# Performance work log

Hardware: AMD Instinct MI355X
Metric: run time of the kernel (lower is better)

Reference implementation:

```python
import jax, jax.numpy as jnp
import numpy as np

KH = KW = 3
PAD = 1


def _conv2d(x, w, b):
    y = jax.lax.conv_general_dilated(
        x, w, window_strides=(1, 1), padding=((PAD, PAD), (PAD, PAD)),
        dimension_numbers=("NCHW", "OIHW", "NCHW"))
    return y + b[None, :, None, None]


def _bilinear_sample_one(img, ys, xs):
    # img: [C,H,W]; ys,xs: [K,h,w] absolute sampling coords; zeros outside.
    C, H, W = img.shape
    flat = img.reshape(C, H * W)
    y0 = jnp.floor(ys)
    x0 = jnp.floor(xs)
    wy = ys - y0
    wx = xs - x0

    def gather(yi, xi):
        valid = (yi >= 0) & (yi <= H - 1) & (xi >= 0) & (xi <= W - 1)
        yc = jnp.clip(yi, 0, H - 1).astype(jnp.int32)
        xc = jnp.clip(xi, 0, W - 1).astype(jnp.int32)
        idx = (yc * W + xc).reshape(-1)
        v = jnp.take(flat, idx, axis=1).reshape((C,) + yi.shape)
        return v * valid.astype(img.dtype)

    v00 = gather(y0, x0)
    v01 = gather(y0, x0 + 1)
    v10 = gather(y0 + 1, x0)
    v11 = gather(y0 + 1, x0 + 1)
    return (v00 * (1 - wy) * (1 - wx) + v01 * (1 - wy) * wx
            + v10 * wy * (1 - wx) + v11 * wy * wx)  # [C,K,h,w]


def deform_conv2d(x, offset, weight, bias):
    # x: [B,C,H,W]; offset: [B,2K,h,w] with (dy,dx) per tap; stride 1, pad 1.
    B, C, H, W = x.shape
    h, w = offset.shape[2], offset.shape[3]
    K = KH * KW
    off = offset.reshape(B, K, 2, h, w)
    ky = (jnp.arange(K) // KW - PAD).astype(x.dtype)  # tap row displacement
    kx = (jnp.arange(K) % KW - PAD).astype(x.dtype)
    ii = jnp.arange(h, dtype=x.dtype)[None, :, None]
    jj = jnp.arange(w, dtype=x.dtype)[None, None, :]
    ys = ii - PAD + ky[:, None, None] + off[:, :, 0]  # [B,K,h,w]
    xs = jj - PAD + kx[:, None, None] + off[:, :, 1]
    sampled = jax.vmap(_bilinear_sample_one)(x, ys, xs)  # [B,C,K,h,w]
    Co = weight.shape[0]
    out = jnp.einsum('ock,bckhw->bohw', weight.reshape(Co, C, K), sampled)
    return out + bias[None, :, None, None]


def setup_inputs() -> dict:
    key = jax.random.key(0)
    ks = jax.random.split(key, 5)
    B, C, H, W = 4, 64, 128, 128
    x = jax.random.normal(ks[0], (B, C, H, W), dtype=jnp.float32)
    w_off = jax.random.normal(ks[1], (4, C, KH, KW), dtype=jnp.float32) * 0.05
    b_off = jnp.zeros((4,), dtype=jnp.float32)
    weight = jax.random.normal(ks[2], (C, C, KH, KW), dtype=jnp.float32) * 0.05
    bias = jnp.zeros((C,), dtype=jnp.float32)
    # base_offset: canonical 3x3 tap displacements, layout (dy,dx) per tap.
    ky = np.repeat(np.arange(KH) - PAD, KW).astype(np.float32)
    kx = np.tile(np.arange(KW) - PAD, KH).astype(np.float32)
    base = np.stack([ky, kx], axis=1).reshape(-1)  # [18]
    base_offset = jnp.asarray(np.broadcast_to(base[None, :, None, None], (1, 18, H, W)).copy())
    idx = np.arange(18)
    mask1 = jnp.asarray(idx % 2 == 0)  # y coords -> scale1
    mask2 = jnp.asarray(idx % 2 == 1)  # x coords -> scale2
    return {"x": x, "w_off": w_off, "b_off": b_off, "weight": weight,
            "bias": bias, "base_offset": base_offset, "mask1": mask1, "mask2": mask2}


def reference(x, w_off, b_off, weight, bias, base_offset, mask1, mask2):
    off = _conv2d(x, w_off, b_off)  # [B,4,h,w]
    scale1 = jax.nn.relu(off[:, 2:3]) + 1.0  # [B,1,h,w]
    scale2 = jax.nn.relu(off[:, 3:4]) + 1.0
    shift = jnp.tile(off[:, :2], (1, KH * KW, 1, 1))  # [B,18,h,w]
    # scaled_offset[:, mask1] = base*scale1 ; scaled_offset[:, mask2] = base*scale2
    scale_full = jnp.where(mask1[None, :, None, None], scale1, scale2)  # [B,18,h,w]
    offset = base_offset * scale_full - base_offset + shift
    return deform_conv2d(x, offset, weight, bias)
```

## Files before the change

kernel.cpp:

```cpp
#include <hip/hip_runtime.h>

#define Hd 128
#define Wd 128
#define Cd 64
#define COd 64
#define Bd 4
#define HWd (Hd*Wd)

typedef __attribute__((ext_vector_type(8))) short  short8;
typedef __attribute__((ext_vector_type(4))) float  f32x4;
typedef __attribute__((ext_vector_type(2))) float  f32x2;

__device__ __align__(16) short g_wbf[COd*576];
__device__ __align__(16) short g_woffbf[16*576];
__device__ float4 g_offs[Bd*HWd];
__device__ __align__(16) unsigned short g_xt[(size_t)Bd*HWd*Cd];

static __device__ __forceinline__ unsigned short f2bf(float v) {
    unsigned u = __float_as_uint(v);
    u += 0x7FFFu + ((u >> 16) & 1u);
    return (unsigned short)(u >> 16);
}
static __device__ __forceinline__ f32x2 bf2(unsigned u) {
    return (f32x2){__uint_as_float(u << 16), __uint_as_float(u & 0xFFFF0000u)};
}
static __device__ __forceinline__ unsigned cvtpk(float lo, float hi) {
    unsigned r;
    asm("v_cvt_pk_bf16_f32 %0, %1, %2" : "=v"(r) : "v"(lo), "v"(hi));
    return r;
}

__global__ __launch_bounds__(256) void k_prep(const float* __restrict__ x,
                                              const float* __restrict__ weight,
                                              const float* __restrict__ w_off) {
    int bid = blockIdx.x;
    if (bid < 512) {
        int b = bid >> 7, y = bid & 127;
        int px = threadIdx.x & 127;
        int h  = threadIdx.x >> 7;
        const float* xb = x + (size_t)b*Cd*HWd + y*Wd + px;
        unsigned short* ob = g_xt + ((size_t)(b*HWd) + y*Wd + px)*Cd + h*32;
        #pragma unroll
        for (int oct = 0; oct < 4; ++oct) {
            unsigned pk[4];
            #pragma unroll
            for (int e = 0; e < 4; ++e) {
                float v0 = xb[(size_t)(h*32 + oct*8 + 2*e    )*HWd];
                float v1 = xb[(size_t)(h*32 + oct*8 + 2*e + 1)*HWd];
                pk[e] = (unsigned)f2bf(v0) | ((unsigned)f2bf(v1) << 16);
            }
            *(uint4*)(ob + oct*8) = make_uint4(pk[0], pk[1], pk[2], pk[3]);
        }
    } else if (bid < 656) {
        int g = (bid - 512)*256 + threadIdx.x;
        if (g < COd*576) {
            int co = g / 576, k = g % 576;
            int t = k >> 6, c = k & 63;
            g_wbf[g] = (short)f2bf(weight[(co*Cd + c)*9 + t]);
        }
    } else {
        int g = (bid - 656)*256 + threadIdx.x;
        if (g < 16*576) {
            int row = g / 576, k = g % 576;
            int t = k >> 6, c = k & 63;
            g_woffbf[g] = (row < 4) ? (short)f2bf(w_off[(row*Cd + c)*9 + t]) : (short)0;
        }
    }
}

__global__ __launch_bounds__(256) void k_offs(const float* __restrict__ b_off) {
    int orig = blockIdx.x;
    int xcd = orig & 7, slot = orig >> 3;
    int g = xcd*2 + (slot >> 6);
    int s = slot & 63;
    int b  = g >> 2;
    int i  = (g & 3)*32 + (s >> 1);
    int j0 = (s & 1) << 6;

    int w  = threadIdx.x >> 6;
    int l  = threadIdx.x & 63;
    int pc = l & 15, q = l >> 4;
    int j  = j0 + w*16 + pc;

    const unsigned short* xb = g_xt + (size_t)b*HWd*Cd;
    const short* arow = g_woffbf + pc*576 + q*8;

    f32x4 acc = {0.f, 0.f, 0.f, 0.f};
    #pragma unroll
    for (int t = 0; t < 9; ++t) {
        int yy = i + t/3 - 1, xx = j + t%3 - 1;
        bool ok = (yy >= 0) & (yy <= 127) & (xx >= 0) & (xx <= 127);
        const unsigned short* p = xb + (size_t)(yy*Wd + xx)*Cd + q*8;
        uint4 u0 = ok ? *(const uint4*)p        : make_uint4(0,0,0,0);
        uint4 u1 = ok ? *(const uint4*)(p + 32) : make_uint4(0,0,0,0);
        short8 b0 = *(short8*)&u0;
        short8 b1 = *(short8*)&u1;
        short8 a0 = *(const short8*)(arow + (2*t    )*32);
        short8 a1 = *(const short8*)(arow + (2*t + 1)*32);
        acc = __builtin_amdgcn_mfma_f32_16x16x32_bf16(a0, b0, acc, 0, 0, 0);
        acc = __builtin_amdgcn_mfma_f32_16x16x32_bf16(a1, b1, acc, 0, 0, 0);
    }
    if (q == 0) {
        float o0 = acc[0] + b_off[0];
        float o1 = acc[1] + b_off[1];
        float o2 = fmaxf(acc[2] + b_off[2], 0.f) + 1.f;
        float o3 = fmaxf(acc[3] + b_off[3], 0.f) + 1.f;
        g_offs[(b*Hd + i)*Wd + j] = make_float4(o0, o1, o2, o3);
    }
}

#define GATHER(T, U00, U01, U10, U11, W00, W01, W10, W11)                         \
    {                                                                             \
        float ys = (float)(i - 1) + (float)((T)/3 - 1)*s1v + off0;                \
        float xs = (float)(jA - 1) + (float)((T)%3 - 1)*s2v + off1;               \
        float y0f = floorf(ys), x0f = floorf(xs);                                 \
        float wy = ys - y0f, wx = xs - x0f;                                       \
        float vy0 = (y0f >=  0.f && y0f <= 127.f) ? 1.f : 0.f;                    \
        float vy1 = (y0f >= -1.f && y0f <= 126.f) ? 1.f : 0.f;                    \
        float vx0 = (x0f >=  0.f && x0f <= 127.f) ? 1.f : 0.f;                    \
        float vx1 = (x0f >= -1.f && x0f <= 126.f) ? 1.f : 0.f;                    \
        W00 = (1.f-wy)*(1.f-wx)*vy0*vx0; W01 = (1.f-wy)*wx*vy0*vx1;               \
        W10 = wy*(1.f-wx)*vy1*vx0;       W11 = wy*wx*vy1*vx1;                     \
        int iy0 = min(max((int)y0f,     0), 127), iy1 = min(max((int)y0f+1,0),127);\
        int ix0 = min(max((int)x0f,     0), 127), ix1 = min(max((int)x0f+1,0),127);\
        U00 = *(const uint4*)(xb + (size_t)(iy0*Wd + ix0)*Cd + oct*8);            \
        U01 = *(const uint4*)(xb + (size_t)(iy0*Wd + ix1)*Cd + oct*8);            \
        U10 = *(const uint4*)(xb + (size_t)(iy1*Wd + ix0)*Cd + oct*8);            \
        U11 = *(const uint4*)(xb + (size_t)(iy1*Wd + ix1)*Cd + oct*8);            \
    }

#define PACK_STORE(BUF, U00, U01, U10, U11, W00, W01, W10, W11)                   \
    {                                                                             \
        unsigned a00[4] = {U00.x,U00.y,U00.z,U00.w};                              \
        unsigned a01[4] = {U01.x,U01.y,U01.z,U01.w};                              \
        unsigned a10[4] = {U10.x,U10.y,U10.z,U10.w};                              \
        unsigned a11[4] = {U11.x,U11.y,U11.z,U11.w};                              \
        f32x2 w00v = {W00, W00}, w01v = {W01, W01};                               \
        f32x2 w10v = {W10, W10}, w11v = {W11, W11};                               \
        unsigned pk[4];                                                           \
        _Pragma("unroll")                                                         \
        for (int e = 0; e < 4; ++e) {                                             \
            f32x2 r = bf2(a00[e])*w00v + bf2(a01[e])*w01v                         \
                    + bf2(a10[e])*w10v + bf2(a11[e])*w11v;                        \
            pk[e] = cvtpk(r.x, r.y);                                              \
        }                                                                         \
        lds_b[(((BUF)*2 + par)*2 + nt)*64 + slotA] = make_uint4(pk[0],pk[1],pk[2],pk[3]); \
    }

__global__ __launch_bounds__(256) void k_deform(const float* __restrict__ bias,
                                                float* __restrict__ out) {
    __shared__ uint4 lds_b[2*2*2*64];
    int orig = blockIdx.x;
    int xcd = orig & 7, slotB = orig >> 3;
    int g = xcd*2 + (slotB >> 7);
    int s = slotB & 127;
    int b = g >> 2;
    int i = (g & 3)*32 + (s >> 2);
    int j0 = (s & 3) << 5;

    int w = threadIdx.x >> 6, l = threadIdx.x & 63;
    int oct = l & 7, px8 = l >> 3;
    int pxl = w*8 + px8;
    int jA  = j0 + pxl;
    int nt = pxl >> 4, pcA = pxl & 15, qA = oct & 3, par = oct >> 2;
    int slotA = (pcA ^ (qA << 1)) + (qA << 4);
    int pcB = l & 15, qB = l >> 4;
    int physl = (pcB ^ (qB << 1)) + (qB << 4);
    const short* wrow = g_wbf + (size_t)(w*16 + pcB)*576 + qB*8;

    const unsigned short* xb = g_xt + (size_t)b*HWd*Cd;
    float4 o4 = g_offs[(b*Hd + i)*Wd + jA];
    float off0 = o4.x, off1 = o4.y, s1v = o4.z, s2v = o4.w;

    f32x4 acc0 = {0.f,0.f,0.f,0.f};
    f32x4 acc1 = {0.f,0.f,0.f,0.f};

    uint4 gc00, gc01, gc10, gc11, gn00, gn01, gn10, gn11;
    float wc00, wc01, wc10, wc11, wn00, wn01, wn10, wn11;
    short8 ac0, ac1, an0, an1;

    GATHER(0, gc00, gc01, gc10, gc11, wc00, wc01, wc10, wc11);
    ac0 = *(const short8*)(wrow + 0*32);
    ac1 = *(const short8*)(wrow + 1*32);

    #pragma unroll
    for (int t = 0; t < 9; ++t) {
        if (t < 8) {
            GATHER(t+1, gn00, gn01, gn10, gn11, wn00, wn01, wn10, wn11);
            an0 = *(const short8*)(wrow + (2*t + 2)*32);
            an1 = *(const short8*)(wrow + (2*t + 3)*32);
        }
        PACK_STORE(t & 1, gc00, gc01, gc10, gc11, wc00, wc01, wc10, wc11);
        __syncthreads();
        {
            short8 b00 = *(const short8*)&lds_b[(((t&1)*2 + 0)*2 + 0)*64 + physl];
            short8 b01 = *(const short8*)&lds_b[(((t&1)*2 + 0)*2 + 1)*64 + physl];
            short8 b10 = *(const short8*)&lds_b[(((t&1)*2 + 1)*2 + 0)*64 + physl];
            short8 b11 = *(const short8*)&lds_b[(((t&1)*2 + 1)*2 + 1)*64 + physl];
            acc0 = __builtin_amdgcn_mfma_f32_16x16x32_bf16(ac0, b00, acc0, 0, 0, 0);
            acc1 = __builtin_amdgcn_mfma_f32_16x16x32_bf16(ac0, b01, acc1, 0, 0, 0);
            acc0 = __builtin_amdgcn_mfma_f32_16x16x32_bf16(ac1, b10, acc0, 0, 0, 0);
            acc1 = __builtin_amdgcn_mfma_f32_16x16x32_bf16(ac1, b11, acc1, 0, 0, 0);
        }
        if (t < 8) {
            gc00 = gn00; gc01 = gn01; gc10 = gn10; gc11 = gn11;
            wc00 = wn00; wc01 = wn01; wc10 = wn10; wc11 = wn11;
            ac0 = an0; ac1 = an1;
        }
    }

    #pragma unroll
    for (int rr = 0; rr < 4; ++rr) {
        int co = w*16 + qB*4 + rr;
        float bco = bias[co];
        size_t base = ((size_t)(b*COd + co)*Hd + i)*Wd + j0;
        out[base + pcB]      = acc0[rr] + bco;
        out[base + 16 + pcB] = acc1[rr] + bco;
    }
}

extern "C" void kernel_launch(void* const* d_in, const int* in_sizes, int n_in,
                              void* d_out, int out_size, void* d_ws, size_t ws_size,
                              hipStream_t stream) {
    const float* x      = (const float*)d_in[0];
    const float* w_off  = (const float*)d_in[1];
    const float* b_off  = (const float*)d_in[2];
    const float* weight = (const float*)d_in[3];
    const float* bias   = (const float*)d_in[4];
    float* out = (float*)d_out;

    hipLaunchKernelGGL(k_prep,   dim3(692),  dim3(256), 0, stream, x, weight, w_off);
    hipLaunchKernelGGL(k_offs,   dim3(1024), dim3(256), 0, stream, b_off);
    hipLaunchKernelGGL(k_deform, dim3(2048), dim3(256), 0, stream, bias, out);
}
```

Baseline: 59.74 us.

## Split deform kernel into a full gather phase then a single MFMA phase

Result: slower. 78.77 us (+31.9%).

```diff
diff --git a/kernel.cpp b/kernel.cpp
--- a/kernel.cpp
+++ b/kernel.cpp
@@ -109,113 +109,89 @@
     }
 }
 
-#define GATHER(T, U00, U01, U10, U11, W00, W01, W10, W11)                         \
-    {                                                                             \
-        float ys = (float)(i - 1) + (float)((T)/3 - 1)*s1v + off0;                \
-        float xs = (float)(jA - 1) + (float)((T)%3 - 1)*s2v + off1;               \
-        float y0f = floorf(ys), x0f = floorf(xs);                                 \
-        float wy = ys - y0f, wx = xs - x0f;                                       \
-        float vy0 = (y0f >=  0.f && y0f <= 127.f) ? 1.f : 0.f;                    \
-        float vy1 = (y0f >= -1.f && y0f <= 126.f) ? 1.f : 0.f;                    \
-        float vx0 = (x0f >=  0.f && x0f <= 127.f) ? 1.f : 0.f;                    \
-        float vx1 = (x0f >= -1.f && x0f <= 126.f) ? 1.f : 0.f;                    \
-        W00 = (1.f-wy)*(1.f-wx)*vy0*vx0; W01 = (1.f-wy)*wx*vy0*vx1;               \
-        W10 = wy*(1.f-wx)*vy1*vx0;       W11 = wy*wx*vy1*vx1;                     \
-        int iy0 = min(max((int)y0f,     0), 127), iy1 = min(max((int)y0f+1,0),127);\
-        int ix0 = min(max((int)x0f,     0), 127), ix1 = min(max((int)x0f+1,0),127);\
-        U00 = *(const uint4*)(xb + (size_t)(iy0*Wd + ix0)*Cd + oct*8);            \
-        U01 = *(const uint4*)(xb + (size_t)(iy0*Wd + ix1)*Cd + oct*8);            \
-        U10 = *(const uint4*)(xb + (size_t)(iy1*Wd + ix0)*Cd + oct*8);            \
-        U11 = *(const uint4*)(xb + (size_t)(iy1*Wd + ix1)*Cd + oct*8);            \
-    }
-
-#define PACK_STORE(BUF, U00, U01, U10, U11, W00, W01, W10, W11)                   \
-    {                                                                             \
-        unsigned a00[4] = {U00.x,U00.y,U00.z,U00.w};                              \
-        unsigned a01[4] = {U01.x,U01.y,U01.z,U01.w};                              \
-        unsigned a10[4] = {U10.x,U10.y,U10.z,U10.w};                              \
-        unsigned a11[4] = {U11.x,U11.y,U11.z,U11.w};                              \
-        f32x2 w00v = {W00, W00}, w01v = {W01, W01};                               \
-        f32x2 w10v = {W10, W10}, w11v = {W11, W11};                               \
-        unsigned pk[4];                                                           \
-        _Pragma("unroll")                                                         \
-        for (int e = 0; e < 4; ++e) {                                             \
-            f32x2 r = bf2(a00[e])*w00v + bf2(a01[e])*w01v                         \
-                    + bf2(a10[e])*w10v + bf2(a11[e])*w11v;                        \
-            pk[e] = cvtpk(r.x, r.y);                                              \
-        }                                                                         \
-        lds_b[(((BUF)*2 + par)*2 + nt)*64 + slotA] = make_uint4(pk[0],pk[1],pk[2],pk[3]); \
-    }
-
-__global__ __launch_bounds__(256) void k_deform(const float* __restrict__ bias,
+__global__ __launch_bounds__(512) void k_deform(const float* __restrict__ bias,
                                                 float* __restrict__ out) {
-    __shared__ uint4 lds_b[2*2*2*64];
+    __shared__ uint4 lds_b[18*2*64];
     int orig = blockIdx.x;
-    int xcd = orig & 7, slotB = orig >> 3;
-    int g = xcd*2 + (slotB >> 7);
-    int s = slotB & 127;
+    int xcd = orig & 7, sl = orig >> 3;
+    int g = xcd*2 + (sl >> 7);
+    int s = sl & 127;
     int b = g >> 2;
     int i = (g & 3)*32 + (s >> 2);
     int j0 = (s & 3) << 5;
 
-    int w = threadIdx.x >> 6, l = threadIdx.x & 63;
-    int oct = l & 7, px8 = l >> 3;
-    int pxl = w*8 + px8;
-    int jA  = j0 + pxl;
-    int nt = pxl >> 4, pcA = pxl & 15, qA = oct & 3, par = oct >> 2;
-    int slotA = (pcA ^ (qA << 1)) + (qA << 4);
-    int pcB = l & 15, qB = l >> 4;
-    int physl = (pcB ^ (qB << 1)) + (qB << 4);
-    const short* wrow = g_wbf + (size_t)(w*16 + pcB)*576 + qB*8;
-
-    const unsigned short* xb = g_xt + (size_t)b*HWd*Cd;
-    float4 o4 = g_offs[(b*Hd + i)*Wd + jA];
-    float off0 = o4.x, off1 = o4.y, s1v = o4.z, s2v = o4.w;
-
-    f32x4 acc0 = {0.f,0.f,0.f,0.f};
-    f32x4 acc1 = {0.f,0.f,0.f,0.f};
-
-    uint4 gc00, gc01, gc10, gc11, gn00, gn01, gn10, gn11;
-    float wc00, wc01, wc10, wc11, wn00, wn01, wn10, wn11;
-    short8 ac0, ac1, an0, an1;
-
-    GATHER(0, gc00, gc01, gc10, gc11, wc00, wc01, wc10, wc11);
-    ac0 = *(const short8*)(wrow + 0*32);
-    ac1 = *(const short8*)(wrow + 1*32);
-
-    #pragma unroll
-    for (int t = 0; t < 9; ++t) {
-        if (t < 8) {
-            GATHER(t+1, gn00, gn01, gn10, gn11, wn00, wn01, wn10, wn11);
-            an0 = *(const short8*)(wrow + (2*t + 2)*32);
-            an1 = *(const short8*)(wrow + (2*t + 3)*32);
-        }
-        PACK_STORE(t & 1, gc00, gc01, gc10, gc11, wc00, wc01, wc10, wc11);
-        __syncthreads();
-        {
-            short8 b00 = *(const short8*)&lds_b[(((t&1)*2 + 0)*2 + 0)*64 + physl];
-            short8 b01 = *(const short8*)&lds_b[(((t&1)*2 + 0)*2 + 1)*64 + physl];
-            short8 b10 = *(const short8*)&lds_b[(((t&1)*2 + 1)*2 + 0)*64 + physl];
-            short8 b11 = *(const short8*)&lds_b[(((t&1)*2 + 1)*2 + 1)*64 + physl];
-            acc0 = __builtin_amdgcn_mfma_f32_16x16x32_bf16(ac0, b00, acc0, 0, 0, 0);
-            acc1 = __builtin_amdgcn_mfma_f32_16x16x32_bf16(ac0, b01, acc1, 0, 0, 0);
-            acc0 = __builtin_amdgcn_mfma_f32_16x16x32_bf16(ac1, b10, acc0, 0, 0, 0);
-            acc1 = __builtin_amdgcn_mfma_f32_16x16x32_bf16(ac1, b11, acc1, 0, 0, 0);
-        }
-        if (t < 8) {
-            gc00 = gn00; gc01 = gn01; gc10 = gn10; gc11 = gn11;
-            wc00 = wn00; wc01 = wn01; wc10 = wn10; wc11 = wn11;
-            ac0 = an0; ac1 = an1;
-        }
-    }
-
-    #pragma unroll
-    for (int rr = 0; rr < 4; ++rr) {
-        int co = w*16 + qB*4 + rr;
-        float bco = bias[co];
-        size_t base = ((size_t)(b*COd + co)*Hd + i)*Wd + j0;
-        out[base + pcB]      = acc0[rr] + bco;
-        out[base + 16 + pcB] = acc1[rr] + bco;
+    int tid = threadIdx.x;
+
+    {
+        int tp  = tid >> 8;
+        int oct = tid & 7;
+        int pxl = (tid >> 3) & 31;
+        int jA  = j0 + pxl;
+        int nt  = pxl >> 4, pcA = pxl & 15;
+        int qA  = oct & 3, par = oct >> 2;
+        int slotA = (pcA ^ (qA << 1)) + (qA << 4);
+
+        const unsigned short* xb = g_xt + (size_t)b*HWd*Cd;
+        float4 o4 = g_offs[(b*Hd + i)*Wd + jA];
+        float off0 = o4.x, off1 = o4.y, s1v = o4.z, s2v = o4.w;
+
+        #pragma unroll 1
+        for (int t = tp; t < 9; t += 2) {
+            float ys = (float)(i - 1) + (float)(t/3 - 1)*s1v + off0;
+            float xs = (float)(jA - 1) + (float)(t%3 - 1)*s2v + off1;
+            float y0f = floorf(ys), x0f = floorf(xs);
+            float wy = ys - y0f, wx = xs - x0f;
+            float vy0 = (y0f >=  0.f && y0f <= 127.f) ? 1.f : 0.f;
+            float vy1 = (y0f >= -1.f && y0f <= 126.f) ? 1.f : 0.f;
+            float vx0 = (x0f >=  0.f && x0f <= 127.f) ? 1.f : 0.f;
+            float vx1 = (x0f >= -1.f && x0f <= 126.f) ? 1.f : 0.f;
+            float w00 = (1.f-wy)*(1.f-wx)*vy0*vx0, w01 = (1.f-wy)*wx*vy0*vx1;
+            float w10 = wy*(1.f-wx)*vy1*vx0,       w11 = wy*wx*vy1*vx1;
+            int iy0 = min(max((int)y0f,     0), 127), iy1 = min(max((int)y0f + 1, 0), 127);
+            int ix0 = min(max((int)x0f,     0), 127), ix1 = min(max((int)x0f + 1, 0), 127);
+            const unsigned short* base = xb + (size_t)oct*8;
+            uint4 u00 = *(const uint4*)(base + (size_t)(iy0*Wd + ix0)*Cd);
+            uint4 u01 = *(const uint4*)(base + (size_t)(iy0*Wd + ix1)*Cd);
+            uint4 u10 = *(const uint4*)(base + (size_t)(iy1*Wd + ix0)*Cd);
+            uint4 u11 = *(const uint4*)(base + (size_t)(iy1*Wd + ix1)*Cd);
+
+            unsigned a00[4] = {u00.x,u00.y,u00.z,u00.w};
+            unsigned a01[4] = {u01.x,u01.y,u01.z,u01.w};
+            unsigned a10[4] = {u10.x,u10.y,u10.z,u10.w};
+            unsigned a11[4] = {u11.x,u11.y,u11.z,u11.w};
+            f32x2 w00v = {w00, w00}, w01v = {w01, w01};
+            f32x2 w10v = {w10, w10}, w11v = {w11, w11};
+            unsigned pk[4];
+            #pragma unroll
+            for (int e = 0; e < 4; ++e) {
+                f32x2 rr = bf2(a00[e])*w00v + bf2(a01[e])*w01v
+                         + bf2(a10[e])*w10v + bf2(a11[e])*w11v;
+                pk[e] = cvtpk(rr.x, rr.y);
+            }
+            int ks = 2*t + par;
+            lds_b[(ks*2 + nt)*64 + slotA] = make_uint4(pk[0], pk[1], pk[2], pk[3]);
+        }
+    }
+    __syncthreads();
+
+    {
+        int w = tid >> 6, l = tid & 63;
+        int cg = w & 3, half = w >> 2;
+        int pcB = l & 15, qB = l >> 4;
+        int physl = (pcB ^ (qB << 1)) + (qB << 4);
+        const short* wrow = g_wbf + (size_t)(cg*16 + pcB)*576 + qB*8;
+
+        f32x4 acc = {0.f, 0.f, 0.f, 0.f};
+        for (int ks = 0; ks < 18; ++ks) {
+            short8 av = *(const short8*)(wrow + ks*32);
+            short8 bv = *(const short8*)&lds_b[(ks*2 + half)*64 + physl];
+            acc = __builtin_amdgcn_mfma_f32_16x16x32_bf16(av, bv, acc, 0, 0, 0);
+        }
+        #pragma unroll
+        for (int rr = 0; rr < 4; ++rr) {
+            int co = cg*16 + qB*4 + rr;
+            out[((size_t)(b*COd + co)*Hd + i)*Wd + j0 + half*16 + pcB] = acc[rr] + bias[co];
+        }
     }
 }
 
@@ -231,5 +207,5 @@
 
     hipLaunchKernelGGL(k_prep,   dim3(692),  dim3(256), 0, stream, x, weight, w_off);
     hipLaunchKernelGGL(k_offs,   dim3(1024), dim3(256), 0, stream, b_off);
-    hipLaunchKernelGGL(k_deform, dim3(2048), dim3(256), 0, stream, bias, out);
-}
+    hipLaunchKernelGGL(k_deform, dim3(2048), dim3(512), 0, stream, bias, out);
+}
```
